# Optimization experiments

Hardware: AMD Instinct MI355X
Metric: run time of the kernel (lower is better)

Reference implementation:

```python
import jax, jax.numpy as jnp
import numpy as np


def _bilinear2d(uv, table):
    """Bilinear lookup with wrap addressing; sigmoid non-linearity applied per
    corner (normalize=True in SpatialGrid2D), matching training-time forward.
    uv: (N,2) in [0,1); table: (U,V,L). Returns (N,L)."""
    U, V, _ = table.shape
    su = uv[:, 0] * U
    sv = uv[:, 1] * V
    u0 = jnp.floor(su)
    v0 = jnp.floor(sv)
    fu = (su - u0)[:, None]  # fractional weights, (N,1)
    fv = (sv - v0)[:, None]
    u0i = jnp.mod(u0.astype(jnp.int32), U)
    v0i = jnp.mod(v0.astype(jnp.int32), V)
    u1i = jnp.mod(u0i + 1, U)
    v1i = jnp.mod(v0i + 1, V)
    t00 = jax.nn.sigmoid(table[u0i, v0i])
    t10 = jax.nn.sigmoid(table[u1i, v0i])
    t01 = jax.nn.sigmoid(table[u0i, v1i])
    t11 = jax.nn.sigmoid(table[u1i, v1i])
    return (t00 * (1 - fu) + t10 * fu) * (1 - fv) + (t01 * (1 - fu) + t11 * fu) * fv


def setup_inputs() -> dict:
    key = jax.random.key(0)
    k1, k2, k3 = jax.random.split(key, 3)
    N = 2048 * 2048  # query points (one per pixel)
    RES = 520        # grid0 resolution from nativeResolution=4096, compression=6
    x = jax.random.uniform(k1, (N, 2), dtype=jnp.float32)
    grid1_table = jax.random.normal(k2, (RES * 4, RES * 4, 2), dtype=jnp.float32)
    grid0_table = jax.random.normal(k3, (RES, RES, 3), dtype=jnp.float32)
    return {"x": x, "grid1_table": grid1_table, "grid0_table": grid0_table}


def reference(x, grid1_table, grid0_table):
    # forward: grid0(grid1(x)) -- chained bilinear indirection lookups
    key = _bilinear2d(x, grid1_table)   # (N,2) indirected uv coords in (0,1)
    return _bilinear2d(key, grid0_table)  # (N,3) decoded RGB
```

## Files before the change

kernel.cpp:

```cpp
#include <hip/hip_runtime.h>
#include <math.h>


typedef float f32x2 __attribute__((ext_vector_type(2)));
typedef float f32x4 __attribute__((ext_vector_type(4)));

__device__ __forceinline__ float mul_rn_nocontract(float a, float b) {
    float r;
    asm("v_mul_f32 %0, %1, %2" : "=v"(r) : "v"(a), "v"(b));
    return r;
}

__device__ __forceinline__ float sigmoid_ref(float t) {
    float e = expf(-t);
    return (float)(1.0 / (1.0 + (double)e));
}

__global__ void __launch_bounds__(256) pack_fused_kernel(
    const float* __restrict__ g1, float* __restrict__ pk, int U1)
{
    int v = blockIdx.x * 256 + threadIdx.x;
    int u = blockIdx.y;
    if (v >= U1) return;
    int v1 = v + 1; if (v1 >= U1) v1 = 0;
    int u1 = u + 1; if (u1 >= U1) u1 = 0;

    const f32x2* g = reinterpret_cast<const f32x2*>(g1);
    size_t ru0 = (size_t)u  * U1;
    size_t ru1 = (size_t)u1 * U1;
    f32x2 t00 = g[ru0 + v];
    f32x2 t01 = g[ru0 + v1];
    f32x2 t10 = g[ru1 + v];
    f32x2 t11 = g[ru1 + v1];

    f32x4 lo, hi;
    lo.x = sigmoid_ref(t00.x); lo.y = sigmoid_ref(t00.y);
    lo.z = sigmoid_ref(t01.x); lo.w = sigmoid_ref(t01.y);
    hi.x = sigmoid_ref(t10.x); hi.y = sigmoid_ref(t10.y);
    hi.z = sigmoid_ref(t11.x); hi.w = sigmoid_ref(t11.y);

    f32x4* o = reinterpret_cast<f32x4*>(pk + (ru0 + v) * 8);
    o[0] = lo;
    o[1] = hi;
}

__global__ void __launch_bounds__(256) sigmoid_table_kernel(
    const float4* __restrict__ in, float4* __restrict__ out, int n4)
{
    int i = blockIdx.x * blockDim.x + threadIdx.x;
    if (i >= n4) return;
    float4 v = in[i];
    float4 r;
    r.x = sigmoid_ref(v.x);
    r.y = sigmoid_ref(v.y);
    r.z = sigmoid_ref(v.z);
    r.w = sigmoid_ref(v.w);
    out[i] = r;
}

__global__ void __launch_bounds__(256) query_packed_kernel(
    const float* __restrict__ x,
    const float* __restrict__ pk,
    const float* __restrict__ s0,
    float* __restrict__ out,
    int N, int U1, int U0)
{
    int i = blockIdx.x * blockDim.x + threadIdx.x;
    if (i >= N) return;

    f32x2 uv = __builtin_nontemporal_load(
        reinterpret_cast<const f32x2*>(x) + i);

    float fU1 = (float)U1;
    float su = mul_rn_nocontract(uv.x, fU1);
    float sv = mul_rn_nocontract(uv.y, fU1);
    float u0f = floorf(su), v0f = floorf(sv);
    float fu = su - u0f;
    float fv = sv - v0f;
    int u0 = (int)u0f % U1; if (u0 < 0) u0 += U1;
    int v0 = (int)v0f % U1; if (v0 < 0) v0 += U1;

    const float4* cell = reinterpret_cast<const float4*>(pk)
                       + (size_t)(u0 * U1 + v0) * 2;
    float4 lo = cell[0];
    float4 hi = cell[1];

    float omfu = 1.0f - fu, omfv = 1.0f - fv;
    float kx = (lo.x * omfu + hi.x * fu) * omfv
             + (lo.z * omfu + hi.z * fu) * fv;
    float ky = (lo.y * omfu + hi.y * fu) * omfv
             + (lo.w * omfu + hi.w * fu) * fv;

    float fU0 = (float)U0;
    float su2 = mul_rn_nocontract(kx, fU0);
    float sv2 = mul_rn_nocontract(ky, fU0);
    float u0f2 = floorf(su2), v0f2 = floorf(sv2);
    float fu2 = su2 - u0f2, fv2 = sv2 - v0f2;
    int p0 = (int)u0f2 % U0; if (p0 < 0) p0 += U0;
    int q0 = (int)v0f2 % U0; if (q0 < 0) q0 += U0;
    int p1 = p0 + 1; if (p1 >= U0) p1 = 0;
    int q1 = q0 + 1; if (q1 >= U0) q1 = 0;
    int b00 = (p0 * U0 + q0) * 3, b10 = (p1 * U0 + q0) * 3;
    int b01 = (p0 * U0 + q1) * 3, b11 = (p1 * U0 + q1) * 3;
    float omfu2 = 1.0f - fu2, omfv2 = 1.0f - fv2;
    float r0 = (s0[b00+0] * omfu2 + s0[b10+0] * fu2) * omfv2
             + (s0[b01+0] * omfu2 + s0[b11+0] * fu2) * fv2;
    float r1 = (s0[b00+1] * omfu2 + s0[b10+1] * fu2) * omfv2
             + (s0[b01+1] * omfu2 + s0[b11+1] * fu2) * fv2;
    float r2 = (s0[b00+2] * omfu2 + s0[b10+2] * fu2) * omfv2
             + (s0[b01+2] * omfu2 + s0[b11+2] * fu2) * fv2;
    out[3*i+0] = r0; out[3*i+1] = r1; out[3*i+2] = r2;
}

__global__ void __launch_bounds__(256) query_kernel_unpadded(
    const float* __restrict__ x,
    const float* __restrict__ s1,
    const float* __restrict__ s0,
    float* __restrict__ out,
    int N, int U1, int U0)
{
    int i = blockIdx.x * blockDim.x + threadIdx.x;
    if (i >= N) return;
    float2 uv = reinterpret_cast<const float2*>(x)[i];
    float fU1 = (float)U1;
    float su = mul_rn_nocontract(uv.x, fU1);
    float sv = mul_rn_nocontract(uv.y, fU1);
    float u0f = floorf(su), v0f = floorf(sv);
    float fu = su - u0f, fv = sv - v0f;
    int u0 = (int)u0f % U1; if (u0 < 0) u0 += U1;
    int v0 = (int)v0f % U1; if (v0 < 0) v0 += U1;
    int u1 = u0 + 1; if (u1 >= U1) u1 = 0;
    int v1 = v0 + 1; if (v1 >= U1) v1 = 0;
    const float2* s1v = reinterpret_cast<const float2*>(s1);
    float2 t00 = s1v[u0 * U1 + v0];
    float2 t10 = s1v[u1 * U1 + v0];
    float2 t01 = s1v[u0 * U1 + v1];
    float2 t11 = s1v[u1 * U1 + v1];
    float omfu = 1.0f - fu, omfv = 1.0f - fv;
    float kx = (t00.x * omfu + t10.x * fu) * omfv + (t01.x * omfu + t11.x * fu) * fv;
    float ky = (t00.y * omfu + t10.y * fu) * omfv + (t01.y * omfu + t11.y * fu) * fv;
    float fU0 = (float)U0;
    float su2 = mul_rn_nocontract(kx, fU0);
    float sv2 = mul_rn_nocontract(ky, fU0);
    float u0f2 = floorf(su2), v0f2 = floorf(sv2);
    float fu2 = su2 - u0f2, fv2 = sv2 - v0f2;
    int p0 = (int)u0f2 % U0; if (p0 < 0) p0 += U0;
    int q0 = (int)v0f2 % U0; if (q0 < 0) q0 += U0;
    int p1 = p0 + 1; if (p1 >= U0) p1 = 0;
    int q1 = q0 + 1; if (q1 >= U0) q1 = 0;
    int b00 = (p0 * U0 + q0) * 3, b10 = (p1 * U0 + q0) * 3;
    int b01 = (p0 * U0 + q1) * 3, b11 = (p1 * U0 + q1) * 3;
    float omfu2 = 1.0f - fu2, omfv2 = 1.0f - fv2;
    float r0 = (s0[b00+0] * omfu2 + s0[b10+0] * fu2) * omfv2
             + (s0[b01+0] * omfu2 + s0[b11+0] * fu2) * fv2;
    float r1 = (s0[b00+1] * omfu2 + s0[b10+1] * fu2) * omfv2
             + (s0[b01+1] * omfu2 + s0[b11+1] * fu2) * fv2;
    float r2 = (s0[b00+2] * omfu2 + s0[b10+2] * fu2) * omfv2
             + (s0[b01+2] * omfu2 + s0[b11+2] * fu2) * fv2;
    out[3*i+0] = r0; out[3*i+1] = r1; out[3*i+2] = r2;
}

__global__ void __launch_bounds__(256) query_kernel_fallback(
    const float* __restrict__ x,
    const float* __restrict__ g1,
    const float* __restrict__ g0,
    float* __restrict__ out,
    int N, int U1, int U0)
{
    int i = blockIdx.x * blockDim.x + threadIdx.x;
    if (i >= N) return;
    float2 uv = reinterpret_cast<const float2*>(x)[i];
    float fU1 = (float)U1;
    float su = mul_rn_nocontract(uv.x, fU1);
    float sv = mul_rn_nocontract(uv.y, fU1);
    float u0f = floorf(su), v0f = floorf(sv);
    float fu = su - u0f, fv = sv - v0f;
    int u0 = (int)u0f % U1; if (u0 < 0) u0 += U1;
    int v0 = (int)v0f % U1; if (v0 < 0) v0 += U1;
    int u1 = u0 + 1; if (u1 >= U1) u1 = 0;
    int v1 = v0 + 1; if (v1 >= U1) v1 = 0;
    const float2* g1v = reinterpret_cast<const float2*>(g1);
    float2 t00 = g1v[u0 * U1 + v0];
    float2 t10 = g1v[u1 * U1 + v0];
    float2 t01 = g1v[u0 * U1 + v1];
    float2 t11 = g1v[u1 * U1 + v1];
    float a00x = sigmoid_ref(t00.x), a00y = sigmoid_ref(t00.y);
    float a10x = sigmoid_ref(t10.x), a10y = sigmoid_ref(t10.y);
    float a01x = sigmoid_ref(t01.x), a01y = sigmoid_ref(t01.y);
    float a11x = sigmoid_ref(t11.x), a11y = sigmoid_ref(t11.y);
    float omfu = 1.0f - fu, omfv = 1.0f - fv;
    float kx = (a00x * omfu + a10x * fu) * omfv + (a01x * omfu + a11x * fu) * fv;
    float ky = (a00y * omfu + a10y * fu) * omfv + (a01y * omfu + a11y * fu) * fv;
    float fU0 = (float)U0;
    float su2 = mul_rn_nocontract(kx, fU0);
    float sv2 = mul_rn_nocontract(ky, fU0);
    float u0f2 = floorf(su2), v0f2 = floorf(sv2);
    float fu2 = su2 - u0f2, fv2 = sv2 - v0f2;
    int p0 = (int)u0f2 % U0; if (p0 < 0) p0 += U0;
    int q0 = (int)v0f2 % U0; if (q0 < 0) q0 += U0;
    int p1 = p0 + 1; if (p1 >= U0) p1 = 0;
    int q1 = q0 + 1; if (q1 >= U0) q1 = 0;
    int b00 = (p0 * U0 + q0) * 3, b10 = (p1 * U0 + q0) * 3;
    int b01 = (p0 * U0 + q1) * 3, b11 = (p1 * U0 + q1) * 3;
    float omfu2 = 1.0f - fu2, omfv2 = 1.0f - fv2;
    float r0 = (sigmoid_ref(g0[b00+0]) * omfu2 + sigmoid_ref(g0[b10+0]) * fu2) * omfv2
             + (sigmoid_ref(g0[b01+0]) * omfu2 + sigmoid_ref(g0[b11+0]) * fu2) * fv2;
    float r1 = (sigmoid_ref(g0[b00+1]) * omfu2 + sigmoid_ref(g0[b10+1]) * fu2) * omfv2
             + (sigmoid_ref(g0[b01+1]) * omfu2 + sigmoid_ref(g0[b11+1]) * fu2) * fv2;
    float r2 = (sigmoid_ref(g0[b00+2]) * omfu2 + sigmoid_ref(g0[b10+2]) * fu2) * omfv2
             + (sigmoid_ref(g0[b01+2]) * omfu2 + sigmoid_ref(g0[b11+2]) * fu2) * fv2;
    out[3*i+0] = r0; out[3*i+1] = r1; out[3*i+2] = r2;
}

extern "C" void kernel_launch(void* const* d_in, const int* in_sizes, int n_in,
                              void* d_out, int out_size, void* d_ws, size_t ws_size,
                              hipStream_t stream) {
    const float* x  = (const float*)d_in[0];
    const float* g1 = (const float*)d_in[1];
    const float* g0 = (const float*)d_in[2];
    float* out = (float*)d_out;

    int N = in_sizes[0] / 2;
    long long n1 = in_sizes[1];
    long long n0 = in_sizes[2];
    int U1 = (int)(sqrt((double)(n1 / 2)) + 0.5);
    int U0 = (int)(sqrt((double)(n0 / 3)) + 0.5);
    long long ncells1 = (long long)U1 * U1;

    int block = 256;
    size_t need_packed = ((size_t)ncells1 * 8 + (size_t)n0) * sizeof(float);
    size_t need_plain  = ((size_t)n1 + (size_t)n0) * sizeof(float);

    if (ws_size >= need_packed && (n0 % 4) == 0) {
        float* pk = (float*)d_ws;
        float* s0 = pk + ncells1 * 8;
        int n0_4 = (int)(n0 / 4);
        dim3 pgrid((U1 + block - 1) / block, U1);
        pack_fused_kernel<<<pgrid, block, 0, stream>>>(g1, pk, U1);
        sigmoid_table_kernel<<<(n0_4 + block - 1) / block, block, 0, stream>>>(
            (const float4*)g0, (float4*)s0, n0_4);
        query_packed_kernel<<<(N + block - 1) / block, block, 0, stream>>>(
            x, pk, s0, out, N, U1, U0);
    } else if (ws_size >= need_plain && (n1 % 4) == 0 && (n0 % 4) == 0) {
        float* s1 = (float*)d_ws;
        float* s0 = s1 + n1;
        int n1_4 = (int)(n1 / 4), n0_4 = (int)(n0 / 4);
        sigmoid_table_kernel<<<(n1_4 + block - 1) / block, block, 0, stream>>>(
            (const float4*)g1, (float4*)s1, n1_4);
        sigmoid_table_kernel<<<(n0_4 + block - 1) / block, block, 0, stream>>>(
            (const float4*)g0, (float4*)s0, n0_4);
        query_kernel_unpadded<<<(N + block - 1) / block, block, 0, stream>>>(
            x, s1, s0, out, N, U1, U0);
    } else {
        query_kernel_fallback<<<(N + block - 1) / block, block, 0, stream>>>(
            x, g1, g0, out, N, U1, U0);
    }
}
```

Measured before the change: 260.4 us.

## Store raw row-pair table and move corner sigmoids into query kernel

Replaces the 8-float per-cell pre-sigmoided corner table with a 4-float raw row-pair table (rows u and u+1), halving the workspace written and read. The query kernel now loads two adjacent row-pair entries and evaluates the eight corner sigmoids itself. This trades memory traffic and pre-pass cost for extra per-query sigmoid arithmetic (double-precision divide) and two loads instead of one contiguous pair.

```diff
diff --git a/kernel.cpp b/kernel.cpp
--- a/kernel.cpp
+++ b/kernel.cpp
@@ -16,32 +16,21 @@
     return (float)(1.0 / (1.0 + (double)e));
 }
 
-__global__ void __launch_bounds__(256) pack_fused_kernel(
-    const float* __restrict__ g1, float* __restrict__ pk, int U1)
+__global__ void __launch_bounds__(256) rowpair_pack_kernel(
+    const float* __restrict__ g1, float* __restrict__ rp, int U1)
 {
     int v = blockIdx.x * 256 + threadIdx.x;
     int u = blockIdx.y;
     if (v >= U1) return;
-    int v1 = v + 1; if (v1 >= U1) v1 = 0;
     int u1 = u + 1; if (u1 >= U1) u1 = 0;
 
     const f32x2* g = reinterpret_cast<const f32x2*>(g1);
-    size_t ru0 = (size_t)u  * U1;
-    size_t ru1 = (size_t)u1 * U1;
-    f32x2 t00 = g[ru0 + v];
-    f32x2 t01 = g[ru0 + v1];
-    f32x2 t10 = g[ru1 + v];
-    f32x2 t11 = g[ru1 + v1];
-
-    f32x4 lo, hi;
-    lo.x = sigmoid_ref(t00.x); lo.y = sigmoid_ref(t00.y);
-    lo.z = sigmoid_ref(t01.x); lo.w = sigmoid_ref(t01.y);
-    hi.x = sigmoid_ref(t10.x); hi.y = sigmoid_ref(t10.y);
-    hi.z = sigmoid_ref(t11.x); hi.w = sigmoid_ref(t11.y);
-
-    f32x4* o = reinterpret_cast<f32x4*>(pk + (ru0 + v) * 8);
-    o[0] = lo;
-    o[1] = hi;
+    f32x2 a = g[(size_t)u  * U1 + v];
+    f32x2 b = g[(size_t)u1 * U1 + v];
+    f32x4 e;
+    e.x = a.x; e.y = a.y; e.z = b.x; e.w = b.y;
+    __builtin_nontemporal_store(
+        e, reinterpret_cast<f32x4*>(rp) + ((size_t)u * U1 + v));
 }
 
 __global__ void __launch_bounds__(256) sigmoid_table_kernel(
@@ -58,9 +47,9 @@
     out[i] = r;
 }
 
-__global__ void __launch_bounds__(256) query_packed_kernel(
+__global__ void __launch_bounds__(256) query_rowpair_kernel(
     const float* __restrict__ x,
-    const float* __restrict__ pk,
+    const float* __restrict__ rp,
     const float* __restrict__ s0,
     float* __restrict__ out,
     int N, int U1, int U0)
@@ -79,17 +68,23 @@
     float fv = sv - v0f;
     int u0 = (int)u0f % U1; if (u0 < 0) u0 += U1;
     int v0 = (int)v0f % U1; if (v0 < 0) v0 += U1;
-
-    const float4* cell = reinterpret_cast<const float4*>(pk)
-                       + (size_t)(u0 * U1 + v0) * 2;
-    float4 lo = cell[0];
-    float4 hi = cell[1];
+    int v1 = v0 + 1; if (v1 >= U1) v1 = 0;
+
+    const f32x4* rpv = reinterpret_cast<const f32x4*>(rp)
+                     + (size_t)u0 * U1;
+    f32x4 e0 = rpv[v0];
+    f32x4 e1 = rpv[v1];
+
+    float a00x = sigmoid_ref(e0.x), a00y = sigmoid_ref(e0.y);
+    float a10x = sigmoid_ref(e0.z), a10y = sigmoid_ref(e0.w);
+    float a01x = sigmoid_ref(e1.x), a01y = sigmoid_ref(e1.y);
+    float a11x = sigmoid_ref(e1.z), a11y = sigmoid_ref(e1.w);
 
     float omfu = 1.0f - fu, omfv = 1.0f - fv;
-    float kx = (lo.x * omfu + hi.x * fu) * omfv
-             + (lo.z * omfu + hi.z * fu) * fv;
-    float ky = (lo.y * omfu + hi.y * fu) * omfv
-             + (lo.w * omfu + hi.w * fu) * fv;
+    float kx = (a00x * omfu + a10x * fu) * omfv
+             + (a01x * omfu + a11x * fu) * fv;
+    float ky = (a00y * omfu + a10y * fu) * omfv
+             + (a01y * omfu + a11y * fu) * fv;
 
     float fU0 = (float)U0;
     float su2 = mul_rn_nocontract(kx, fU0);
@@ -228,19 +223,19 @@
     long long ncells1 = (long long)U1 * U1;
 
     int block = 256;
-    size_t need_packed = ((size_t)ncells1 * 8 + (size_t)n0) * sizeof(float);
-    size_t need_plain  = ((size_t)n1 + (size_t)n0) * sizeof(float);
-
-    if (ws_size >= need_packed && (n0 % 4) == 0) {
-        float* pk = (float*)d_ws;
-        float* s0 = pk + ncells1 * 8;
+    size_t need_rowpair = ((size_t)ncells1 * 4 + (size_t)n0) * sizeof(float);
+    size_t need_plain   = ((size_t)n1 + (size_t)n0) * sizeof(float);
+
+    if (ws_size >= need_rowpair && (n0 % 4) == 0) {
+        float* rp = (float*)d_ws;
+        float* s0 = rp + ncells1 * 4;
         int n0_4 = (int)(n0 / 4);
         dim3 pgrid((U1 + block - 1) / block, U1);
-        pack_fused_kernel<<<pgrid, block, 0, stream>>>(g1, pk, U1);
+        rowpair_pack_kernel<<<pgrid, block, 0, stream>>>(g1, rp, U1);
         sigmoid_table_kernel<<<(n0_4 + block - 1) / block, block, 0, stream>>>(
             (const float4*)g0, (float4*)s0, n0_4);
-        query_packed_kernel<<<(N + block - 1) / block, block, 0, stream>>>(
-            x, pk, s0, out, N, U1, U0);
+        query_rowpair_kernel<<<(N + block - 1) / block, block, 0, stream>>>(
+            x, rp, s0, out, N, U1, U0);
     } else if (ws_size >= need_plain && (n1 % 4) == 0 && (n0 % 4) == 0) {
         float* s1 = (float*)d_ws;
         float* s0 = s1 + n1;
```

New measurement: 251.8 us. 3.3% less time.
